# Performance work log

Hardware: AMD Instinct MI355X
Metric: run time of the kernel (lower is better)

Reference implementation:

```python
import jax, jax.numpy as jnp
import numpy as np

B, N, D, H = 8, 1024, 768, 12
HD = D // H  # 64


def setup_inputs() -> dict:
    key = jax.random.key(0)
    ks = jax.random.split(key, 10)
    input_graph = jax.random.normal(ks[0], (B, N, D), dtype=jnp.float32)
    u = jax.random.uniform(ks[1], (B, N, N), dtype=jnp.float32)
    keep = jax.random.uniform(ks[2], (B, N, N)) < 0.15
    adj = jnp.where(keep, u, 0.0)
    s = 1.0 / np.sqrt(D)
    Wq = jax.random.normal(ks[3], (D, D), dtype=jnp.float32) * s
    bq = jnp.zeros((D,), dtype=jnp.float32)
    Wk = jax.random.normal(ks[4], (D, D), dtype=jnp.float32) * s
    bk = jnp.zeros((D,), dtype=jnp.float32)
    Wv = jax.random.normal(ks[5], (D, D), dtype=jnp.float32) * s
    bv = jnp.zeros((D,), dtype=jnp.float32)
    beta = jnp.asarray(0.1, dtype=jnp.float32)
    return {"input_graph": input_graph, "adj": adj, "Wq": Wq, "bq": bq,
            "Wk": Wk, "bk": bk, "Wv": Wv, "bv": bv, "beta": beta}


def _split_heads(x):
    # [B,N,D] -> [B,H,N,HD]
    b, n, _ = x.shape
    return x.reshape(b, n, H, HD).transpose(0, 2, 1, 3)


def reference(input_graph, adj, Wq, bq, Wk, bk, Wv, bv, beta):
    q = _split_heads(input_graph @ Wq + bq)  # [B,H,N,HD]
    k = _split_heads(input_graph @ Wk + bk)
    v = _split_heads(input_graph @ Wv + bv)
    scores = jnp.einsum('bhqd,bhkd->bhqk', q, k) / jnp.sqrt(jnp.asarray(HD, input_graph.dtype))
    adj_e = adj[:, None, :, :]  # [B,1,N,N]
    scores = scores + beta * adj_e
    scores = jnp.where(adj_e > 0, scores, jnp.asarray(-9e15, scores.dtype))
    probs = jax.nn.softmax(scores, axis=-1)
    out = jnp.einsum('bhqk,bhkd->bhqd', probs, v)  # [B,H,N,HD]
    return out.transpose(0, 2, 1, 3).reshape(input_graph.shape[0], input_graph.shape[1], D)
```

## Files before the change

### kernel.cpp

```cpp
#include <hip/hip_runtime.h>

#define B_ 8
#define N_ 1024
#define D_ 768
#define H_ 12
#define HD_ 64

#define LOG2E 1.4426950408889634f

typedef __attribute__((ext_vector_type(8))) short bf16x8;
typedef __attribute__((ext_vector_type(4))) short short4_t;
typedef __attribute__((ext_vector_type(4))) float f32x4;
typedef __attribute__((ext_vector_type(2))) unsigned int u32x2;
typedef unsigned int u32;

__device__ __forceinline__ short f2bf(float f) {
  union { float f; unsigned u; } v; v.f = f;
  unsigned u = v.u;
  unsigned r = u + 0x7fffu + ((u >> 16) & 1u);
  return (short)(r >> 16);
}
__device__ __forceinline__ float bf2f(short s) {
  union { unsigned u; float f; } v;
  v.u = ((unsigned)(unsigned short)s) << 16;
  return v.f;
}
__device__ __forceinline__ u32 fbits(float f) {
  union { float f; u32 u; } v; v.f = f; return v.u;
}
__device__ __forceinline__ float bpermf(int srclane, float x) {
  union { float f; int i; } v; v.f = x;
  union { int i; float f; } r;
  r.i = __builtin_amdgcn_ds_bpermute(srclane * 4, v.i);
  return r.f;
}

__device__ __forceinline__ void gload_lds16(const void* g, void* l) {
  __builtin_amdgcn_global_load_lds((const __attribute__((address_space(1))) u32*)g,
                                   (__attribute__((address_space(3))) u32*)l, 16, 0, 0);
}

__global__ void cvt_x_kernel(const float* __restrict__ X, short* __restrict__ Xb) {
  int i = (blockIdx.x * 256 + threadIdx.x) * 8;
  float4 a = *(const float4*)(X + i);
  float4 b = *(const float4*)(X + i + 4);
  bf16x8 o;
  o[0] = f2bf(a.x); o[1] = f2bf(a.y); o[2] = f2bf(a.z); o[3] = f2bf(a.w);
  o[4] = f2bf(b.x); o[5] = f2bf(b.y); o[6] = f2bf(b.z); o[7] = f2bf(b.w);
  *(bf16x8*)(Xb + i) = o;
}

__global__ void cvt_w_kernel(const float* __restrict__ Wq, const float* __restrict__ Wk,
                             const float* __restrict__ Wv, short* __restrict__ Wt3) {
  const float* W = blockIdx.z == 0 ? Wq : (blockIdx.z == 1 ? Wk : Wv);
  short* O = Wt3 + (size_t)blockIdx.z * D_ * D_;
  __shared__ float t[32][33];
  int n0 = blockIdx.x * 32, k0 = blockIdx.y * 32;
  int tx = threadIdx.x, ty = threadIdx.y;
#pragma unroll
  for (int j = 0; j < 4; j++)
    t[ty + 8 * j][tx] = W[(size_t)(k0 + ty + 8 * j) * D_ + n0 + tx];
  __syncthreads();
#pragma unroll
  for (int j = 0; j < 4; j++)
    O[(size_t)(n0 + ty + 8 * j) * D_ + k0 + tx] = f2bf(t[tx][ty + 8 * j]);
}

__global__ __launch_bounds__(256)
void madj_kernel(const float* __restrict__ adj, const float* __restrict__ beta_p,
                 short* __restrict__ madjF) {
  const int qt = blockIdx.x, kt = blockIdx.y, b = blockIdx.z;
  const int tid = threadIdx.x;
  const float b2 = beta_p[0] * LOG2E;
  const float MASKV = -9.0e15f * LOG2E;

  __shared__ float Lt[64][68];
  {
    const int row = tid >> 2, cs = (tid & 3) * 16;
    const float* ap = adj + ((size_t)b * N_ + qt * 64 + row) * (size_t)N_ + kt * 64 + cs;
#pragma unroll
    for (int j = 0; j < 4; j++)
      *(float4*)&Lt[row][cs + 4 * j] = *(const float4*)(ap + 4 * j);
  }
  __syncthreads();

  const int lane = tid & 63, w = tid >> 6;
  const int l15 = lane & 15, lg = lane >> 4;
  const int q = 16 * w + l15;
  short vals[16];
#pragma unroll
  for (int cb = 0; cb < 4; cb++) {
    float4 a4 = *(const float4*)&Lt[q][16 * cb + 4 * lg];
    float av[4] = {a4.x, a4.y, a4.z, a4.w};
#pragma unroll
    for (int r = 0; r < 4; r++) {
      float a = av[r];
      vals[cb * 4 + r] = f2bf((a > 0.f) ? b2 * a : MASKV);
    }
  }
  short* o = madjF + (((size_t)(b * 16 + qt) * 16 + kt) * 256 + tid) * 16;
  bf16x8 lo, hi;
#pragma unroll
  for (int j = 0; j < 8; j++) { lo[j] = vals[j]; hi[j] = vals[8 + j]; }
  *(bf16x8*)o = lo;
  *(bf16x8*)(o + 8) = hi;
}

__global__ __launch_bounds__(256, 4)
void qkv_gemm_kernel(const short* __restrict__ Xb, const short* __restrict__ Wt3,
                     const float* __restrict__ bq, const float* __restrict__ bk,
                     const float* __restrict__ bv, short* __restrict__ QKV) {
  const int z = blockIdx.z;
  const short* Wt = Wt3 + (size_t)z * D_ * D_;
  const float* bias = z == 0 ? bq : (z == 1 ? bk : bv);
  short* C = QKV + (size_t)z * (B_ * N_) * D_;
  const float alpha = (z == 0) ? 0.125f * LOG2E : 1.0f;

  const int m0 = blockIdx.x * 128;
  const int n0 = blockIdx.y * 128;
  const int tid = threadIdx.x;
  const int lane = tid & 63;
  const int wid = tid >> 6;
  const int wr = (wid >> 1) * 64;
  const int wc = (wid & 1) * 64;
  const int l15 = lane & 15;
  const int lg = lane >> 4;

  __shared__ short At[128][32];
  __shared__ short Bt[128][32];

  f32x4 acc[4][4];
#pragma unroll
  for (int m = 0; m < 4; m++)
#pragma unroll
    for (int n = 0; n < 4; n++)
      acc[m][n] = (f32x4){0.f, 0.f, 0.f, 0.f};

  const int srow_l = lane >> 2;
  const int sc8 = (((lane & 3) ^ ((lane >> 2) & 3)) * 8);

  for (int k0 = 0; k0 < D_; k0 += 32) {
    __syncthreads();
#pragma unroll
    for (int p = 0; p < 2; p++) {
      const int row = (wid + 4 * p) * 16 + srow_l;
      gload_lds16(Xb + (size_t)(m0 + row) * D_ + k0 + sc8,
                  ((short*)At) + (size_t)(wid + 4 * p) * 512);
      gload_lds16(Wt + (size_t)(n0 + row) * D_ + k0 + sc8,
                  ((short*)Bt) + (size_t)(wid + 4 * p) * 512);
    }
    __syncthreads();

    bf16x8 af[4], bfr[4];
#pragma unroll
    for (int m = 0; m < 4; m++) {
      const int row = wr + m * 16 + l15;
      af[m] = *(const bf16x8*)&At[row][(lg ^ (l15 & 3)) * 8];
    }
#pragma unroll
    for (int n = 0; n < 4; n++) {
      const int row = wc + n * 16 + l15;
      bfr[n] = *(const bf16x8*)&Bt[row][(lg ^ (l15 & 3)) * 8];
    }
#pragma unroll
    for (int m = 0; m < 4; m++)
#pragma unroll
      for (int n = 0; n < 4; n++)
        acc[m][n] = __builtin_amdgcn_mfma_f32_16x16x32_bf16(af[m], bfr[n], acc[m][n], 0, 0, 0);
  }

#pragma unroll
  for (int n = 0; n < 4; n++) {
    const int col = n0 + wc + n * 16 + l15;
    const float bval = bias[col];
#pragma unroll
    for (int m = 0; m < 4; m++) {
#pragma unroll
      for (int r = 0; r < 4; r++) {
        const int row = m0 + wr + m * 16 + 4 * lg + r;
        C[(size_t)row * D_ + col] = f2bf((acc[m][n][r] + bval) * alpha);
      }
    }
  }
}

__global__ __launch_bounds__(256)
void vT_kernel(const short* __restrict__ Vb, short* __restrict__ VTg) {
  const int nt = blockIdx.x, h = blockIdx.y, b = blockIdx.z;
  const int tid = threadIdx.x;
  __shared__ short st[64][68];
  const int n0 = nt * 64;
  {
    const int row = tid >> 2, c = (tid & 3) * 16;
    const short* p = Vb + ((size_t)b * N_ + n0 + row) * D_ + h * HD_ + c;
    *(bf16x8*)&st[row][c] = *(const bf16x8*)p;
    *(bf16x8*)&st[row][c + 8] = *(const bf16x8*)(p + 8);
  }
  __syncthreads();
  {
    const int d = tid >> 2, nb = (tid & 3) * 16;
    bf16x8 o0, o1;
#pragma unroll
    for (int i = 0; i < 8; i++) { o0[i] = st[nb + i][d]; o1[i] = st[nb + 8 + i][d]; }
    short* q = VTg + ((size_t)(b * H_ + h) * HD_ + d) * N_ + n0 + nb;
    *(bf16x8*)q = o0;
    *(bf16x8*)(q + 8) = o1;
  }
}

__global__ __launch_bounds__(256, 4)
void attn_kernel(const short* __restrict__ QKV, const short* __restrict__ VTg,
                 const short* __restrict__ madjF, float* __restrict__ out) {
  const short* Qb = QKV;
  const short* Kb = QKV + (size_t)(B_ * N_) * D_;

  const int wg = blockIdx.x;
  const int swz = (wg & 7) * 192 + (wg >> 3);
  const int qt = swz & 15;
  const int h = (swz >> 4) % 12;
  const int b = swz / 192;

  const int tid = threadIdx.x;
  const int lane = tid & 63;
  const int w = tid >> 6;
  const int l15 = lane & 15;
  const int lg = lane >> 4;

  const int q0 = qt * 64;
  const size_t seq0 = (size_t)b * N_;
  const int hc = h * HD_;

  __shared__ short Kt[64][64];
  __shared__ short VTt[64][64];
  __shared__ short Pt[4][16][64];

  bf16x8 qf[2];
  {
    const short* qp = Qb + (seq0 + q0 + 16 * w + l15) * (size_t)D_ + hc + 8 * lg;
    qf[0] = *(const bf16x8*)qp;
    qf[1] = *(const bf16x8*)(qp + 32);
  }

  f32x4 acc[4];
#pragma unroll
  for (int cb = 0; cb < 4; cb++) acc[cb] = (f32x4){0.f, 0.f, 0.f, 0.f};
  float m_ = -__builtin_inff();
  float l_ = 0.f;

  const int krow = 16 * w + (lane >> 3);
  const int kc8 = ((lane & 7) ^ (lane >> 3)) * 8;
  const short* kg = Kb + (seq0 + krow) * (size_t)D_ + hc + kc8;
  const short* vg = VTg + ((size_t)(b * H_ + h) * HD_ + krow) * N_ + kc8;
  const short* mg = madjF + ((size_t)(b * 16 + qt) * 16) * 4096 + tid * 16;

  const int sw2 = (l15 & 7) << 1;
  char* ptrow = (char*)&Pt[w][l15][0];

  for (int kt = 0; kt < 16; kt++) {
    const int k0 = kt * 64;
    __syncthreads();

    gload_lds16(kg + (size_t)k0 * D_, ((short*)Kt) + (size_t)w * 1024);
    gload_lds16(kg + (size_t)(k0 + 8) * D_, ((short*)Kt) + (size_t)w * 1024 + 512);
    gload_lds16(vg + k0, ((short*)VTt) + (size_t)w * 1024);
    gload_lds16(vg + k0 + 8 * (size_t)N_, ((short*)VTt) + (size_t)w * 1024 + 512);
    bf16x8 mlo = *(const bf16x8*)(mg + (size_t)kt * 4096);
    bf16x8 mhi = *(const bf16x8*)(mg + (size_t)kt * 4096 + 8);

    __syncthreads();

    f32x4 s[4];
#pragma unroll
    for (int cb = 0; cb < 4; cb++) {
      f32x4 c;
#pragma unroll
      for (int r = 0; r < 4; r++)
        c[r] = bf2f(cb < 2 ? mlo[(cb & 1) * 4 + r] : mhi[(cb & 1) * 4 + r]);
      const int swk = l15 & 7;
      bf16x8 kf0 = *(const bf16x8*)&Kt[cb * 16 + l15][(lg ^ swk) * 8];
      bf16x8 kf1 = *(const bf16x8*)&Kt[cb * 16 + l15][((lg + 4) ^ swk) * 8];
      c = __builtin_amdgcn_mfma_f32_16x16x32_bf16(kf0, qf[0], c, 0, 0, 0);
      s[cb] = __builtin_amdgcn_mfma_f32_16x16x32_bf16(kf1, qf[1], c, 0, 0, 0);
    }

    float tm = fmaxf(fmaxf(fmaxf(s[0][0], s[0][1]), fmaxf(s[0][2], s[0][3])),
                     fmaxf(fmaxf(s[1][0], s[1][1]), fmaxf(s[1][2], s[1][3])));
    float tm2 = fmaxf(fmaxf(fmaxf(s[2][0], s[2][1]), fmaxf(s[2][2], s[2][3])),
                      fmaxf(fmaxf(s[3][0], s[3][1]), fmaxf(s[3][2], s[3][3])));
    tm = fmaxf(tm, tm2);
    tm = fmaxf(tm, __shfl_xor(tm, 16));
    tm = fmaxf(tm, __shfl_xor(tm, 32));

    if (!__all(tm <= m_ + 8.f)) {
      const float mnew = fmaxf(m_, tm);
      const float sc2 = __builtin_exp2f(m_ - mnew);
      m_ = mnew;
      l_ *= sc2;
      float scr[4];
#pragma unroll
      for (int r = 0; r < 4; r++) scr[r] = bpermf(4 * lg + r, sc2);
#pragma unroll
      for (int cb = 0; cb < 4; cb++)
#pragma unroll
        for (int r = 0; r < 4; r++) acc[cb][r] *= scr[r];
    }

    float ps = 0.f;
    u32 pk[8];
#pragma unroll
    for (int cb = 0; cb < 4; cb++) {
#pragma unroll
      for (int rp = 0; rp < 2; rp++) {
        const float p0 = __builtin_exp2f(s[cb][2 * rp] - m_);
        const float p1 = __builtin_exp2f(s[cb][2 * rp + 1] - m_);
        ps += p0 + p1;
        pk[cb * 2 + rp] =
            __builtin_amdgcn_perm(fbits(p1) + 0x8000u, fbits(p0) + 0x8000u, 0x07060302u);
      }
    }
    ps += __shfl_xor(ps, 16);
    ps += __shfl_xor(ps, 32);
    l_ += ps;

#pragma unroll
    for (int cb = 0; cb < 4; cb++) {
      u32x2 wv = {pk[2 * cb], pk[2 * cb + 1]};
      *(u32x2*)(ptrow + (((4 * cb + lg) ^ sw2) << 3)) = wv;
    }

#pragma unroll
    for (int ks = 0; ks < 2; ks++) {
      bf16x8 pa = *(const bf16x8*)(ptrow + ((((lg << 1) + 8 * ks) ^ sw2) << 3));
#pragma unroll
      for (int cb = 0; cb < 4; cb++) {
        const int row = cb * 16 + l15;
        bf16x8 vb = *(const bf16x8*)&VTt[row][((lg + 4 * ks) ^ (row & 7)) * 8];
        acc[cb] = __builtin_amdgcn_mfma_f32_16x16x32_bf16(pa, vb, acc[cb], 0, 0, 0);
      }
    }
  }

  float inv[4];
#pragma unroll
  for (int r = 0; r < 4; r++) inv[r] = 1.f / bpermf(4 * lg + r, l_);
#pragma unroll
  for (int cb = 0; cb < 4; cb++) {
#pragma unroll
    for (int r = 0; r < 4; r++) {
      out[(seq0 + q0 + 16 * w + 4 * lg + r) * (size_t)D_ + hc + cb * 16 + l15] =
          acc[cb][r] * inv[r];
    }
  }
}

extern "C" void kernel_launch(void* const* d_in, const int* in_sizes, int n_in,
                              void* d_out, int out_size, void* d_ws, size_t ws_size,
                              hipStream_t stream) {
  const float* X    = (const float*)d_in[0];
  const float* adj  = (const float*)d_in[1];
  const float* Wq   = (const float*)d_in[2];
  const float* bq   = (const float*)d_in[3];
  const float* Wk   = (const float*)d_in[4];
  const float* bk   = (const float*)d_in[5];
  const float* Wv   = (const float*)d_in[6];
  const float* bv   = (const float*)d_in[7];
  const float* beta = (const float*)d_in[8];
  float* out = (float*)d_out;

  short* Xb    = (short*)d_ws;
  short* Wt3   = Xb + (size_t)(B_ * N_) * D_;
  short* QKV   = Wt3 + 3 * (size_t)D_ * D_;
  short* madjF = QKV + 3 * (size_t)(B_ * N_) * D_;
  short* VTg   = Xb;

  cvt_x_kernel<<<dim3((B_ * N_ * D_) / (256 * 8)), 256, 0, stream>>>(X, Xb);
  cvt_w_kernel<<<dim3(24, 24, 3), dim3(32, 8), 0, stream>>>(Wq, Wk, Wv, Wt3);
  madj_kernel<<<dim3(16, 16, 8), 256, 0, stream>>>(adj, beta, madjF);
  qkv_gemm_kernel<<<dim3(64, 6, 3), 256, 0, stream>>>(Xb, Wt3, bq, bk, bv, QKV);
  vT_kernel<<<dim3(16, 12, 8), 256, 0, stream>>>(QKV + 2 * (size_t)(B_ * N_) * D_, VTg);
  attn_kernel<<<dim3(1536), 256, 0, stream>>>(QKV, VTg, madjF, out);
}
```

Before: 135.0 us.

## Double-buffer LDS tiles in QKV GEMM and attention, use packed bf16 convert

```diff
diff --git a/kernel.cpp b/kernel.cpp
--- a/kernel.cpp
+++ b/kernel.cpp
@@ -25,14 +25,19 @@
   v.u = ((unsigned)(unsigned short)s) << 16;
   return v.f;
 }
-__device__ __forceinline__ u32 fbits(float f) {
-  union { float f; u32 u; } v; v.f = f; return v.u;
-}
 __device__ __forceinline__ float bpermf(int srclane, float x) {
   union { float f; int i; } v; v.f = x;
   union { int i; float f; } r;
   r.i = __builtin_amdgcn_ds_bpermute(srclane * 4, v.i);
   return r.f;
+}
+__device__ __forceinline__ float max3f(float a, float b, float c) {
+  return fmaxf(fmaxf(a, b), c);
+}
+__device__ __forceinline__ u32 cvtpk(float a, float b) {
+  u32 r;
+  asm("v_cvt_pk_bf16_f32 %0, %1, %2" : "=v"(r) : "v"(a), "v"(b));
+  return r;
 }
 
 __device__ __forceinline__ void gload_lds16(const void* g, void* l) {
@@ -126,8 +131,8 @@
   const int l15 = lane & 15;
   const int lg = lane >> 4;
 
-  __shared__ short At[128][32];
-  __shared__ short Bt[128][32];
+  __shared__ short At[2][128][32];
+  __shared__ short Bt[2][128][32];
 
   f32x4 acc[4][4];
 #pragma unroll
@@ -138,29 +143,35 @@
 
   const int srow_l = lane >> 2;
   const int sc8 = (((lane & 3) ^ ((lane >> 2) & 3)) * 8);
-
+  const short* ag = Xb + (size_t)(m0 + wid * 16 + srow_l) * D_ + sc8;
+  const short* bg = Wt + (size_t)(n0 + wid * 16 + srow_l) * D_ + sc8;
+
+  auto stage = [&](int bi, int k0) {
+#pragma unroll
+    for (int p = 0; p < 2; p++) {
+      gload_lds16(ag + (size_t)(64 * p) * D_ + k0,
+                  ((short*)At[bi]) + (size_t)(wid + 4 * p) * 512);
+      gload_lds16(bg + (size_t)(64 * p) * D_ + k0,
+                  ((short*)Bt[bi]) + (size_t)(wid + 4 * p) * 512);
+    }
+  };
+
+  stage(0, 0);
   for (int k0 = 0; k0 < D_; k0 += 32) {
+    const int cur = (k0 >> 5) & 1;
     __syncthreads();
-#pragma unroll
-    for (int p = 0; p < 2; p++) {
-      const int row = (wid + 4 * p) * 16 + srow_l;
-      gload_lds16(Xb + (size_t)(m0 + row) * D_ + k0 + sc8,
-                  ((short*)At) + (size_t)(wid + 4 * p) * 512);
-      gload_lds16(Wt + (size_t)(n0 + row) * D_ + k0 + sc8,
-                  ((short*)Bt) + (size_t)(wid + 4 * p) * 512);
-    }
-    __syncthreads();
+    if (k0 + 32 < D_) stage(cur ^ 1, k0 + 32);
 
     bf16x8 af[4], bfr[4];
 #pragma unroll
     for (int m = 0; m < 4; m++) {
       const int row = wr + m * 16 + l15;
-      af[m] = *(const bf16x8*)&At[row][(lg ^ (l15 & 3)) * 8];
+      af[m] = *(const bf16x8*)&At[cur][row][(lg ^ (l15 & 3)) * 8];
     }
 #pragma unroll
     for (int n = 0; n < 4; n++) {
       const int row = wc + n * 16 + l15;
-      bfr[n] = *(const bf16x8*)&Bt[row][(lg ^ (l15 & 3)) * 8];
+      bfr[n] = *(const bf16x8*)&Bt[cur][row][(lg ^ (l15 & 3)) * 8];
     }
 #pragma unroll
     for (int m = 0; m < 4; m++)
@@ -230,8 +241,8 @@
   const size_t seq0 = (size_t)b * N_;
   const int hc = h * HD_;
 
-  __shared__ short Kt[64][64];
-  __shared__ short VTt[64][64];
+  __shared__ short Kt[2][64][64];
+  __shared__ short VTt[2][64][64];
   __shared__ short Pt[4][16][64];
 
   bf16x8 qf[2];
@@ -256,18 +267,25 @@
   const int sw2 = (l15 & 7) << 1;
   char* ptrow = (char*)&Pt[w][l15][0];
 
+  auto stage = [&](int bi, int kt) {
+    const int k0 = kt * 64;
+    gload_lds16(kg + (size_t)k0 * D_, ((short*)Kt[bi]) + (size_t)w * 1024);
+    gload_lds16(kg + (size_t)(k0 + 8) * D_, ((short*)Kt[bi]) + (size_t)w * 1024 + 512);
+    gload_lds16(vg + k0, ((short*)VTt[bi]) + (size_t)w * 1024);
+    gload_lds16(vg + k0 + 8 * (size_t)N_, ((short*)VTt[bi]) + (size_t)w * 1024 + 512);
+  };
+
+  stage(0, 0);
+  bf16x8 mlo = *(const bf16x8*)mg;
+  bf16x8 mhi = *(const bf16x8*)(mg + 8);
+
   for (int kt = 0; kt < 16; kt++) {
-    const int k0 = kt * 64;
+    const int cur = kt & 1;
     __syncthreads();
-
-    gload_lds16(kg + (size_t)k0 * D_, ((short*)Kt) + (size_t)w * 1024);
-    gload_lds16(kg + (size_t)(k0 + 8) * D_, ((short*)Kt) + (size_t)w * 1024 + 512);
-    gload_lds16(vg + k0, ((short*)VTt) + (size_t)w * 1024);
-    gload_lds16(vg + k0 + 8 * (size_t)N_, ((short*)VTt) + (size_t)w * 1024 + 512);
-    bf16x8 mlo = *(const bf16x8*)(mg + (size_t)kt * 4096);
-    bf16x8 mhi = *(const bf16x8*)(mg + (size_t)kt * 4096 + 8);
-
-    __syncthreads();
+    if (kt < 15) stage(cur ^ 1, kt + 1);
+    const int ktn = kt < 15 ? kt + 1 : 15;
+    bf16x8 mlo2 = *(const bf16x8*)(mg + (size_t)ktn * 4096);
+    bf16x8 mhi2 = *(const bf16x8*)(mg + (size_t)ktn * 4096 + 8);
 
     f32x4 s[4];
 #pragma unroll
@@ -277,16 +295,18 @@
       for (int r = 0; r < 4; r++)
         c[r] = bf2f(cb < 2 ? mlo[(cb & 1) * 4 + r] : mhi[(cb & 1) * 4 + r]);
       const int swk = l15 & 7;
-      bf16x8 kf0 = *(const bf16x8*)&Kt[cb * 16 + l15][(lg ^ swk) * 8];
-      bf16x8 kf1 = *(const bf16x8*)&Kt[cb * 16 + l15][((lg + 4) ^ swk) * 8];
+      bf16x8 kf0 = *(const bf16x8*)&Kt[cur][cb * 16 + l15][(lg ^ swk) * 8];
+      bf16x8 kf1 = *(const bf16x8*)&Kt[cur][cb * 16 + l15][((lg + 4) ^ swk) * 8];
       c = __builtin_amdgcn_mfma_f32_16x16x32_bf16(kf0, qf[0], c, 0, 0, 0);
       s[cb] = __builtin_amdgcn_mfma_f32_16x16x32_bf16(kf1, qf[1], c, 0, 0, 0);
     }
-
-    float tm = fmaxf(fmaxf(fmaxf(s[0][0], s[0][1]), fmaxf(s[0][2], s[0][3])),
-                     fmaxf(fmaxf(s[1][0], s[1][1]), fmaxf(s[1][2], s[1][3])));
-    float tm2 = fmaxf(fmaxf(fmaxf(s[2][0], s[2][1]), fmaxf(s[2][2], s[2][3])),
-                      fmaxf(fmaxf(s[3][0], s[3][1]), fmaxf(s[3][2], s[3][3])));
+    mlo = mlo2; mhi = mhi2;
+
+    float tm = max3f(max3f(s[0][0], s[0][1], s[0][2]),
+                     max3f(s[0][3], s[1][0], s[1][1]),
+                     max3f(s[1][2], s[1][3], s[2][0]));
+    float tm2 = max3f(max3f(s[2][1], s[2][2], s[2][3]),
+                      max3f(s[3][0], s[3][1], s[3][2]), s[3][3]);
     tm = fmaxf(tm, tm2);
     tm = fmaxf(tm, __shfl_xor(tm, 16));
     tm = fmaxf(tm, __shfl_xor(tm, 32));
@@ -314,8 +334,7 @@
         const float p0 = __builtin_exp2f(s[cb][2 * rp] - m_);
         const float p1 = __builtin_exp2f(s[cb][2 * rp + 1] - m_);
         ps += p0 + p1;
-        pk[cb * 2 + rp] =
-            __builtin_amdgcn_perm(fbits(p1) + 0x8000u, fbits(p0) + 0x8000u, 0x07060302u);
+        pk[cb * 2 + rp] = cvtpk(p0, p1);
       }
     }
     ps += __shfl_xor(ps, 16);
@@ -334,7 +353,7 @@
 #pragma unroll
       for (int cb = 0; cb < 4; cb++) {
         const int row = cb * 16 + l15;
-        bf16x8 vb = *(const bf16x8*)&VTt[row][((lg + 4 * ks) ^ (row & 7)) * 8];
+        bf16x8 vb = *(const bf16x8*)&VTt[cur][row][((lg + 4 * ks) ^ (row & 7)) * 8];
         acc[cb] = __builtin_amdgcn_mfma_f32_16x16x32_bf16(pa, vb, acc[cb], 0, 0, 0);
       }
     }
```

New measurement: 131.2 us. 2.8% less time.
